# Kernel tuning notes

Hardware: AMD Instinct MI355X
Metric: run time of the kernel (lower is better)

The kernel has to match this reference:

```python
import jax, jax.numpy as jnp
import numpy as np

B, N, D, H = 4, 256, 256, 8
HD = D // H
DFF = 4 * D
EPS = 1e-5


def setup_inputs() -> dict:
    key = jax.random.key(0)
    ks = jax.random.split(key, 12)
    s = 0.02
    p = lambda k, shape: (jax.random.normal(k, shape, jnp.float32) * s)
    return dict(
        h=jax.random.normal(ks[0], (B, N, D), jnp.float32),
        e=jax.random.normal(ks[1], (B, N, N, D), jnp.float32),
        We=p(ks[2], (D, D)), be=jnp.zeros((D,), jnp.float32),
        Ws=p(ks[3], (D, D)), bs=jnp.zeros((D,), jnp.float32),
        Wd=p(ks[4], (D, D)), bd=jnp.zeros((D,), jnp.float32),
        Wb=p(ks[5], (D, H)), bb=jnp.zeros((H,), jnp.float32),
        ln1_g=jnp.ones((D,), jnp.float32), ln1_b=jnp.zeros((D,), jnp.float32),
        Wqkv=p(ks[6], (D, 3 * D)), bqkv=jnp.zeros((3 * D,), jnp.float32),
        Wo=p(ks[7], (D, D)), bo=jnp.zeros((D,), jnp.float32),
        ln2_g=jnp.ones((D,), jnp.float32), ln2_b=jnp.zeros((D,), jnp.float32),
        W1=p(ks[8], (D, DFF)), b1=jnp.zeros((DFF,), jnp.float32),
        W2=p(ks[9], (DFF, D)), b2=jnp.zeros((D,), jnp.float32),
    )


def _ln(x, g, b):
    m = jnp.mean(x, axis=-1, keepdims=True)
    v = jnp.mean((x - m) ** 2, axis=-1, keepdims=True)
    return (x - m) * jax.lax.rsqrt(v + EPS) * g + b


def reference(h, e, We, be, Ws, bs, Wd, bd, Wb, bb, ln1_g, ln1_b,
              Wqkv, bqkv, Wo, bo, ln2_g, ln2_b, W1, b1, W2, b2):
    # Edge update: broadcast-add of src/dst node projections + ReLU over [B,N,N,D]
    e_new = jax.nn.relu(e @ We + be
                        + (h @ Ws + bs)[:, :, None, :]   # src -> unsqueeze(2)
                        + (h @ Wd + bd)[:, None, :, :])  # dst -> unsqueeze(1)
    # Per-head additive attention bias [B,H,N,N]
    bias = jnp.einsum('bijd,dh->bhij', e_new, Wb) + bb[None, :, None, None]
    # Pre-LN self-attention with additive bias (torch MHA, eval mode)
    x = _ln(h, ln1_g, ln1_b)
    qkv = x @ Wqkv + bqkv
    q, k, v = jnp.split(qkv, 3, axis=-1)
    q = q.reshape(B, N, H, HD)
    k = k.reshape(B, N, H, HD)
    v = v.reshape(B, N, H, HD)
    scores = jnp.einsum('bihd,bjhd->bhij', q, k) / np.float32(np.sqrt(HD)) + bias
    attn = jax.nn.softmax(scores, axis=-1)
    o = jnp.einsum('bhij,bjhd->bihd', attn, v).reshape(B, N, D)
    h1 = h + (o @ Wo + bo)
    # Pre-LN FFN (exact GELU, as torch nn.GELU default)
    y = _ln(h1, ln2_g, ln2_b)
    h2 = h1 + (jax.nn.gelu(y @ W1 + b1, approximate=False) @ W2 + b2)
    return (h2, e_new)
```

## Files before the change

kernel.cpp:

```cpp
#include <hip/hip_runtime.h>
#include <math.h>

#define EPS 1e-5f

typedef __attribute__((ext_vector_type(4))) float floatx4;
typedef __attribute__((ext_vector_type(8))) short shortx8;

__device__ __forceinline__ unsigned short f2bf(float f){
  union { float f; unsigned u; } v; v.f = f;
  unsigned r = v.u + 0x7FFFu + ((v.u >> 16) & 1u);
  return (unsigned short)(r >> 16);
}
__device__ __forceinline__ float bf2f(unsigned short s){
  union { unsigned u; float f; } v; v.u = ((unsigned)s) << 16;
  return v.f;
}

__global__ __launch_bounds__(256) void k_prep(const float* __restrict__ We,
                                              unsigned short* __restrict__ WeT){
  int n = blockIdx.x, k = threadIdx.x;
  WeT[n*256 + k] = f2bf(We[k*256 + n]);
}

__global__ __launch_bounds__(256) void k_st(
    const float* __restrict__ h, const float* __restrict__ Ws, const float* __restrict__ bs,
    const float* __restrict__ be, const float* __restrict__ Wd, const float* __restrict__ bd,
    float* __restrict__ S, float* __restrict__ T)
{
  __shared__ float x[4][256];
  int t = threadIdx.x;
  int row0 = blockIdx.x*4;
  int which = blockIdx.y;
#pragma unroll
  for (int r=0;r<4;r++) x[r][t] = h[(row0+r)*256 + t];
  __syncthreads();
  const float* W = which ? Wd : Ws;
  float bv = which ? bd[t] : (bs[t] + be[t]);
  float acc[4] = {bv,bv,bv,bv};
  for (int k=0;k<256;k++){
    float wv = W[k*256 + t];
#pragma unroll
    for (int r=0;r<4;r++) acc[r] += x[r][k]*wv;
  }
  float* outp = which ? T : S;
#pragma unroll
  for (int r=0;r<4;r++) outp[(row0+r)*256 + t] = acc[r];
}

__global__ __launch_bounds__(256) void k_edge(
    const float* __restrict__ e, const unsigned short* __restrict__ WeT,
    const float* __restrict__ S, const float* __restrict__ T,
    const float* __restrict__ Wb, const float* __restrict__ bbv,
    float* __restrict__ eo, float* __restrict__ bias)
{
  __shared__ __align__(16) unsigned short smem[16896];
  __shared__ float sbuf[256];
  __shared__ __align__(16) unsigned short WbT[16*256];
  unsigned short* As = smem;
  unsigned short* Bs = smem + 2560;
  unsigned short* En = smem;

  const int tid = threadIdx.x;
  const int blk = blockIdx.x;
  const int jt = blk & 3;
  const int i  = (blk >> 2) & 255;
  const int b  = blk >> 10;
  const int j0 = jt * 64;
  const int w = tid >> 6, l = tid & 63;
  const int lrow = l & 15, quad = l >> 4;

  sbuf[tid] = S[((b << 8) + i) * 256 + tid];
  {
    const float* wbp = Wb + tid * 8;
    float4 w0 = *(const float4*)wbp;
    float4 w1 = *(const float4*)(wbp + 4);
    WbT[0*256 + tid] = f2bf(w0.x);
    WbT[1*256 + tid] = f2bf(w0.y);
    WbT[2*256 + tid] = f2bf(w0.z);
    WbT[3*256 + tid] = f2bf(w0.w);
    WbT[4*256 + tid] = f2bf(w1.x);
    WbT[5*256 + tid] = f2bf(w1.y);
    WbT[6*256 + tid] = f2bf(w1.z);
    WbT[7*256 + tid] = f2bf(w1.w);
#pragma unroll
    for (int hh = 8; hh < 16; hh++) WbT[hh*256 + tid] = 0;
  }

  floatx4 acc[16];
#pragma unroll
  for (int t = 0; t < 16; t++) acc[t] = (floatx4){0.f,0.f,0.f,0.f};

  const float* eBase = e + ((size_t)((b*256 + i)*256 + j0)) * 256;

  for (int c = 0; c < 8; c++){
    const int k0 = c * 32;
    __syncthreads();
#pragma unroll
    for (int s = 0; s < 2; s++){
      int f = tid + s*256;
      int r = f >> 3, q = f & 7;
      float4 v = *(const float4*)(eBase + r*256 + k0 + q*4);
      unsigned short* dst = As + r*40 + q*4;
      dst[0]=f2bf(v.x); dst[1]=f2bf(v.y); dst[2]=f2bf(v.z); dst[3]=f2bf(v.w);
    }
#pragma unroll
    for (int s = 0; s < 4; s++){
      int f = tid + s*256;
      int n = f >> 2, seg = f & 3;
      uint4 v = *(const uint4*)(WeT + n*256 + k0 + seg*8);
      *(uint4*)(Bs + n*40 + seg*8) = v;
    }
    __syncthreads();
    shortx8 af = *(const shortx8*)(As + (w*16 + lrow)*40 + quad*8);
#pragma unroll
    for (int t = 0; t < 16; t++){
      shortx8 bfrag = *(const shortx8*)(Bs + (t*16 + lrow)*40 + quad*8);
      acc[t] = __builtin_amdgcn_mfma_f32_16x16x32_bf16(af, bfrag, acc[t], 0, 0, 0);
    }
  }
  __syncthreads();
  const float* Tb = T + (size_t)(b*256 + j0) * 256;
#pragma unroll
  for (int reg = 0; reg < 4; reg++){
    int rloc = w*16 + quad*4 + reg;
    const float* Trow = Tb + rloc*256;
#pragma unroll
    for (int t = 0; t < 16; t++){
      int col = t*16 + lrow;
      float v = acc[t][reg] + sbuf[col] + Trow[col];
      v = fmaxf(v, 0.f);
      En[rloc*264 + col] = f2bf(v);
    }
  }
  __syncthreads();
  float* eop = eo + ((size_t)((b*256 + i)*256 + j0)) * 256;
#pragma unroll
  for (int s = 0; s < 16; s++){
    int fi = tid + s*256;
    int r = fi >> 6, c4 = fi & 63;
    const unsigned short* src = En + r*264 + c4*4;
    float4 v = { bf2f(src[0]), bf2f(src[1]), bf2f(src[2]), bf2f(src[3]) };
    *(float4*)(eop + r*256 + c4*4) = v;
  }
  floatx4 accb = (floatx4){0.f,0.f,0.f,0.f};
#pragma unroll
  for (int c = 0; c < 8; c++){
    int k0 = c*32;
    shortx8 af = *(const shortx8*)(En + (w*16 + lrow)*264 + k0 + quad*8);
    shortx8 bfrag = *(const shortx8*)(WbT + lrow*256 + k0 + quad*8);
    accb = __builtin_amdgcn_mfma_f32_16x16x32_bf16(af, bfrag, accb, 0, 0, 0);
  }
  if (lrow < 8){
    float bv = bbv[lrow];
    float* bp = bias + ((size_t)((b*8 + lrow)*256 + i)) * 256;
    int jb = j0 + w*16 + quad*4;
#pragma unroll
    for (int r = 0; r < 4; r++) bp[jb + r] = accb[r] + bv;
  }
}

__global__ __launch_bounds__(256) void k_ln1_qkv(
    const float* __restrict__ h, const float* __restrict__ g1, const float* __restrict__ b1l,
    const float* __restrict__ Wq, const float* __restrict__ bq,
    float* __restrict__ Q, float* __restrict__ K, float* __restrict__ V)
{
  __shared__ float x[4][256];
  __shared__ float red[256];
  __shared__ float mred[4], vred[4];
  int t = threadIdx.x;
  int row0 = blockIdx.x*4;
  int b = row0 >> 8, i0 = row0 & 255;
#pragma unroll
  for (int r=0;r<4;r++) x[r][t] = h[(row0+r)*256 + t];
  __syncthreads();
  int rr = t>>6, seg = t&63;
  const float* xr = x[rr];
  red[t] = xr[seg*4]+xr[seg*4+1]+xr[seg*4+2]+xr[seg*4+3];
  __syncthreads();
  for (int s=32;s>0;s>>=1){ if(seg<s) red[t]+=red[t+s]; __syncthreads(); }
  if (t<4) mred[t] = red[t*64]*(1.f/256.f);
  __syncthreads();
  float m_r = mred[rr];
  float d0=xr[seg*4]-m_r, d1=xr[seg*4+1]-m_r, d2=xr[seg*4+2]-m_r, d3=xr[seg*4+3]-m_r;
  red[t]=d0*d0+d1*d1+d2*d2+d3*d3;
  __syncthreads();
  for (int s=32;s>0;s>>=1){ if(seg<s) red[t]+=red[t+s]; __syncthreads(); }
  if (t<4) vred[t] = rsqrtf(red[t*64]*(1.f/256.f) + EPS);
  __syncthreads();
  float xn[4];
#pragma unroll
  for (int r=0;r<4;r++) xn[r] = (x[r][t]-mred[r])*vred[r]*g1[t] + b1l[t];
  __syncthreads();
#pragma unroll
  for (int r=0;r<4;r++) x[r][t] = xn[r];
  __syncthreads();
  float a0[4], a1[4], a2[4];
#pragma unroll
  for (int r=0;r<4;r++){ a0[r]=bq[t]; a1[r]=bq[t+256]; a2[r]=bq[t+512]; }
  for (int k=0;k<256;k++){
    float x0=x[0][k], x1=x[1][k], x2=x[2][k], x3=x[3][k];
    float w0=Wq[k*768+t], w1=Wq[k*768+t+256], w2=Wq[k*768+t+512];
    a0[0]+=x0*w0; a0[1]+=x1*w0; a0[2]+=x2*w0; a0[3]+=x3*w0;
    a1[0]+=x0*w1; a1[1]+=x1*w1; a1[2]+=x2*w1; a1[3]+=x3*w1;
    a2[0]+=x0*w2; a2[1]+=x1*w2; a2[2]+=x2*w2; a2[3]+=x3*w2;
  }
  int hd = t&31, hed = t>>5;
#pragma unroll
  for (int r=0;r<4;r++){
    int idx = ((b*8 + hed)*256 + (i0+r))*32 + hd;
    Q[idx] = a0[r]; K[idx] = a1[r]; V[idx] = a2[r];
  }
}

__global__ __launch_bounds__(256) void k_attn(
    const float* __restrict__ Q, const float* __restrict__ K, const float* __restrict__ V,
    const float* __restrict__ bias, float* __restrict__ O)
{
  __shared__ float ksl[256*33];
  __shared__ float q[32];
  __shared__ float sc[256];
  __shared__ float red[256];
  __shared__ float part[8*33];
  int t = threadIdx.x;
  int i = blockIdx.x & 255, bh = blockIdx.x >> 8;
  const float* Kb = K + bh*8192;
  const float* Vb = V + bh*8192;
  if (t < 32) q[t] = Q[(bh*256 + i)*32 + t];
#pragma unroll
  for (int s=0;s<8;s++){
    int f = t + s*256;
    int row = f >> 3, seg = f & 7;
    float4 v = ((const float4*)Kb)[f];
    int base = row*33 + seg*4;
    ksl[base]=v.x; ksl[base+1]=v.y; ksl[base+2]=v.z; ksl[base+3]=v.w;
  }
  __syncthreads();
  float a = 0.f;
  const float* kr = ksl + t*33;
#pragma unroll
  for (int d=0; d<32; d++) a += q[d]*kr[d];
  float sv = a*0.17677669529663687f + bias[((size_t)(bh*256 + i))*256 + t];
  red[t] = sv;
  __syncthreads();
  for (int s=128;s>0;s>>=1){ if (t<s) red[t] = fmaxf(red[t], red[t+s]); __syncthreads(); }
  float mx = red[0];
  __syncthreads();
  float p = expf(sv - mx);
  sc[t] = p; red[t] = p;
  __syncthreads();
  for (int s=128;s>0;s>>=1){ if (t<s) red[t] += red[t+s]; __syncthreads(); }
  float inv = 1.f/red[0];
  int hd = t & 31, grp = t >> 5;
  float oa = 0.f;
  const float* vb2 = Vb + grp*32*32;
#pragma unroll
  for (int jj=0;jj<32;jj++) oa += sc[grp*32+jj] * vb2[jj*32 + hd];
  part[grp*33 + hd] = oa;
  __syncthreads();
  if (t < 32){
    float o = 0.f;
#pragma unroll
    for (int gg=0; gg<8; gg++) o += part[gg*33 + t];
    int b = bh >> 3, hh = bh & 7;
    O[((b*256 + i)*256) + hh*32 + t] = o * inv;
  }
}

__global__ __launch_bounds__(256) void k_oproj_ln2(
    const float* __restrict__ O, const float* __restrict__ Wo, const float* __restrict__ bo,
    const float* __restrict__ h, const float* __restrict__ g2, const float* __restrict__ b2l,
    float* __restrict__ h1, float* __restrict__ y)
{
  __shared__ float x[4][256];
  __shared__ float hh[4][256];
  __shared__ float red[256];
  __shared__ float mred[4], vred[4];
  int t = threadIdx.x;
  int row0 = blockIdx.x * 4;
#pragma unroll
  for (int r=0;r<4;r++) x[r][t] = O[(row0+r)*256 + t];
  __syncthreads();
  float acc[4];
#pragma unroll
  for (int r=0;r<4;r++) acc[r] = bo[t];
  for (int k=0;k<256;k++){
    float wv = Wo[k*256 + t];
#pragma unroll
    for (int r=0;r<4;r++) acc[r] += x[r][k]*wv;
  }
#pragma unroll
  for (int r=0;r<4;r++){
    float hv = h[(row0+r)*256 + t] + acc[r];
    hh[r][t] = hv;
    h1[(row0+r)*256 + t] = hv;
  }
  __syncthreads();
  int rr = t>>6, seg = t&63;
  const float* hr = hh[rr];
  red[t] = hr[seg*4]+hr[seg*4+1]+hr[seg*4+2]+hr[seg*4+3];
  __syncthreads();
  for (int s=32;s>0;s>>=1){ if (seg<s) red[t]+=red[t+s]; __syncthreads(); }
  if (t<4) mred[t] = red[t*64]*(1.f/256.f);
  __syncthreads();
  float m_r = mred[rr];
  float d0=hr[seg*4]-m_r, d1=hr[seg*4+1]-m_r, d2=hr[seg*4+2]-m_r, d3=hr[seg*4+3]-m_r;
  red[t] = d0*d0+d1*d1+d2*d2+d3*d3;
  __syncthreads();
  for (int s=32;s>0;s>>=1){ if (seg<s) red[t]+=red[t+s]; __syncthreads(); }
  if (t<4) vred[t] = rsqrtf(red[t*64]*(1.f/256.f) + EPS);
  __syncthreads();
#pragma unroll
  for (int r=0;r<4;r++)
    y[(row0+r)*256 + t] = (hh[r][t]-mred[r])*vred[r]*g2[t] + b2l[t];
}

__global__ __launch_bounds__(256) void k_ffn1(
    const float* __restrict__ y, const float* __restrict__ W1, const float* __restrict__ b1,
    float* __restrict__ G)
{
  __shared__ float x[4][256];
  int t = threadIdx.x;
  int row0 = blockIdx.x*4;
#pragma unroll
  for (int r=0;r<4;r++) x[r][t] = y[(row0+r)*256 + t];
  __syncthreads();
  float acc[4][4];
#pragma unroll
  for (int c=0;c<4;c++){
    float bv = b1[t + c*256];
#pragma unroll
    for (int r=0;r<4;r++) acc[c][r] = bv;
  }
  for (int k=0;k<256;k++){
    float x0=x[0][k],x1=x[1][k],x2=x[2][k],x3=x[3][k];
#pragma unroll
    for (int c=0;c<4;c++){
      float wv = W1[k*1024 + t + c*256];
      acc[c][0]+=x0*wv; acc[c][1]+=x1*wv; acc[c][2]+=x2*wv; acc[c][3]+=x3*wv;
    }
  }
#pragma unroll
  for (int c=0;c<4;c++){
#pragma unroll
    for (int r=0;r<4;r++){
      float v = acc[c][r];
      float ge = 0.5f*v*(1.f + erff(v*0.70710678118654752f));
      G[(row0+r)*1024 + t + c*256] = ge;
    }
  }
}

__global__ __launch_bounds__(256) void k_ffn2(
    const float* __restrict__ G, const float* __restrict__ W2, const float* __restrict__ b2,
    const float* __restrict__ h1, float* __restrict__ out)
{
  __shared__ float g[4*1024];
  int t = threadIdx.x;
  int row0 = blockIdx.x*4;
  const float4* gl = (const float4*)(G + (size_t)row0*1024);
  float4* gs = (float4*)g;
#pragma unroll
  for (int s=0;s<4;s++) gs[t + s*256] = gl[t + s*256];
  __syncthreads();
  float acc[4];
#pragma unroll
  for (int r=0;r<4;r++) acc[r] = b2[t];
  for (int k=0;k<1024;k++){
    float wv = W2[k*256 + t];
#pragma unroll
    for (int r=0;r<4;r++) acc[r] += g[r*1024 + k]*wv;
  }
#pragma unroll
  for (int r=0;r<4;r++) out[(row0+r)*256 + t] = h1[(row0+r)*256 + t] + acc[r];
}

extern "C" void kernel_launch(void* const* d_in, const int* in_sizes, int n_in,
                              void* d_out, int out_size, void* d_ws, size_t ws_size,
                              hipStream_t stream)
{
  (void)in_sizes; (void)n_in; (void)out_size; (void)ws_size;
  const float* h    = (const float*)d_in[0];
  const float* e    = (const float*)d_in[1];
  const float* We   = (const float*)d_in[2];
  const float* be   = (const float*)d_in[3];
  const float* Ws   = (const float*)d_in[4];
  const float* bs   = (const float*)d_in[5];
  const float* Wd   = (const float*)d_in[6];
  const float* bd   = (const float*)d_in[7];
  const float* Wb   = (const float*)d_in[8];
  const float* bb   = (const float*)d_in[9];
  const float* g1   = (const float*)d_in[10];
  const float* b1l  = (const float*)d_in[11];
  const float* Wqkv = (const float*)d_in[12];
  const float* bqkv = (const float*)d_in[13];
  const float* Wo   = (const float*)d_in[14];
  const float* bo   = (const float*)d_in[15];
  const float* g2   = (const float*)d_in[16];
  const float* b2l  = (const float*)d_in[17];
  const float* W1   = (const float*)d_in[18];
  const float* b1f  = (const float*)d_in[19];
  const float* W2   = (const float*)d_in[20];
  const float* b2f  = (const float*)d_in[21];

  float* out   = (float*)d_out;
  float* h2_o  = out;
  float* e_o   = out + 262144;

  float* wsf = (float*)d_ws;
  unsigned short* WeT = (unsigned short*)d_ws;
  float* S_   = wsf + 32768;
  float* T_   = wsf + 294912;
  float* bias = wsf + 557056;
  float* Q_   = wsf + 2654208;
  float* K_   = wsf + 2916352;
  float* V_   = wsf + 3178496;
  float* O_   = wsf + 3440640;
  float* h1_  = wsf + 3702784;
  float* y_   = wsf + 3964928;
  float* G_   = wsf + 4227072;

  k_prep    <<<dim3(256),    dim3(256), 0, stream>>>(We, WeT);
  k_st      <<<dim3(256, 2), dim3(256), 0, stream>>>(h, Ws, bs, be, Wd, bd, S_, T_);
  k_edge    <<<dim3(4096),   dim3(256), 0, stream>>>(e, WeT, S_, T_, Wb, bb, e_o, bias);
  k_ln1_qkv <<<dim3(256),    dim3(256), 0, stream>>>(h, g1, b1l, Wqkv, bqkv, Q_, K_, V_);
  k_attn    <<<dim3(8192),   dim3(256), 0, stream>>>(Q_, K_, V_, bias, O_);
  k_oproj_ln2<<<dim3(256),   dim3(256), 0, stream>>>(O_, Wo, bo, h, g2, b2l, h1_, y_);
  k_ffn1    <<<dim3(256),    dim3(256), 0, stream>>>(y_, W1, b1f, G_);
  k_ffn2    <<<dim3(256),    dim3(256), 0, stream>>>(G_, W2, b2f, h1_, h2_o);
}
```

Baseline: 753.4 us.

## Move all node GEMMs to bf16 MFMA, fuse FFN chain, prefetch edge tiles

Transposes every weight matrix to bf16 in a single prep kernel. The S/T/QKV projections move onto MFMA in one fused front kernel that also does LN1. Attention is rewritten as one block per 32 query rows, using bf16 Q/K/V^T and MFMA for both QK^T and PV. The o-projection, LN2, FFN1+GELU and FFN2 are fused into one back kernel, and the edge GEMM now register-prefetches the next K-chunk. This cuts launches, scalar FP32 GEMM loops and intermediate global traffic, at the cost of more bf16 rounding and a small 64-block grid for the back kernel.

```diff
diff --git a/kernel.cpp b/kernel.cpp
--- a/kernel.cpp
+++ b/kernel.cpp
@@ -16,46 +16,140 @@
   return v.f;
 }
 
-__global__ __launch_bounds__(256) void k_prep(const float* __restrict__ We,
-                                              unsigned short* __restrict__ WeT){
-  int n = blockIdx.x, k = threadIdx.x;
-  WeT[n*256 + k] = f2bf(We[k*256 + n]);
-}
-
-__global__ __launch_bounds__(256) void k_st(
-    const float* __restrict__ h, const float* __restrict__ Ws, const float* __restrict__ bs,
-    const float* __restrict__ be, const float* __restrict__ Wd, const float* __restrict__ bd,
-    float* __restrict__ S, float* __restrict__ T)
+__global__ __launch_bounds__(256) void k_prep(
+    const float* __restrict__ We, const float* __restrict__ Ws, const float* __restrict__ Wd,
+    const float* __restrict__ Wqkv, const float* __restrict__ Wo, const float* __restrict__ W1,
+    const float* __restrict__ W2, const float* __restrict__ Wb,
+    unsigned short* __restrict__ WeT, unsigned short* __restrict__ WsT,
+    unsigned short* __restrict__ WdT, unsigned short* __restrict__ WqkvT,
+    unsigned short* __restrict__ WoT, unsigned short* __restrict__ W1T,
+    unsigned short* __restrict__ W2T, unsigned short* __restrict__ WbT16)
 {
-  __shared__ float x[4][256];
-  int t = threadIdx.x;
-  int row0 = blockIdx.x*4;
-  int which = blockIdx.y;
-#pragma unroll
-  for (int r=0;r<4;r++) x[r][t] = h[(row0+r)*256 + t];
-  __syncthreads();
-  const float* W = which ? Wd : Ws;
-  float bv = which ? bd[t] : (bs[t] + be[t]);
-  float acc[4] = {bv,bv,bv,bv};
-  for (int k=0;k<256;k++){
-    float wv = W[k*256 + t];
-#pragma unroll
-    for (int r=0;r<4;r++) acc[r] += x[r][k]*wv;
-  }
-  float* outp = which ? T : S;
-#pragma unroll
-  for (int r=0;r<4;r++) outp[(row0+r)*256 + t] = acc[r];
+  const int blk = blockIdx.x, tid = threadIdx.x;
+  if (blk == 240){
+#pragma unroll
+    for (int hh=0; hh<8; hh++) WbT16[hh*256+tid] = f2bf(Wb[tid*8+hh]);
+#pragma unroll
+    for (int hh=8; hh<16; hh++) WbT16[hh*256+tid] = 0;
+    return;
+  }
+  const float* src; unsigned short* dst; int K, N, t;
+  if (blk < 16)      { src=We;   dst=WeT;   K=256;  N=256;  t=blk; }
+  else if (blk < 32) { src=Ws;   dst=WsT;   K=256;  N=256;  t=blk-16; }
+  else if (blk < 48) { src=Wd;   dst=WdT;   K=256;  N=256;  t=blk-32; }
+  else if (blk < 96) { src=Wqkv; dst=WqkvT; K=256;  N=768;  t=blk-48; }
+  else if (blk < 112){ src=Wo;   dst=WoT;   K=256;  N=256;  t=blk-96; }
+  else if (blk < 176){ src=W1;   dst=W1T;   K=256;  N=1024; t=blk-112; }
+  else               { src=W2;   dst=W2T;   K=1024; N=256;  t=blk-176; }
+  const int tpr = N >> 6;
+  const int k0 = (t / tpr) << 6, n0 = (t % tpr) << 6;
+  __shared__ float tile[64][65];
+#pragma unroll
+  for (int s=0;s<16;s++){ int f=tid+(s<<8); int r=f>>6, c=f&63;
+    tile[r][c] = src[(size_t)(k0+r)*N + n0 + c]; }
+  __syncthreads();
+#pragma unroll
+  for (int s=0;s<16;s++){ int f=tid+(s<<8); int r=f>>6, c=f&63;
+    dst[(size_t)(n0+r)*K + k0 + c] = f2bf(tile[c][r]); }
+}
+
+__global__ __launch_bounds__(256) void k_front(
+  const float* __restrict__ h, const float* __restrict__ g1, const float* __restrict__ b1l,
+  const float* __restrict__ bs, const float* __restrict__ be, const float* __restrict__ bd,
+  const float* __restrict__ bqkv,
+  const unsigned short* __restrict__ WsT, const unsigned short* __restrict__ WdT,
+  const unsigned short* __restrict__ WqkvT,
+  float* __restrict__ S, float* __restrict__ T,
+  unsigned short* __restrict__ Qb, unsigned short* __restrict__ Kb,
+  unsigned short* __restrict__ VTb)
+{
+  __shared__ float hs[16][256];
+  __shared__ __align__(16) unsigned short xa[16*264];
+  __shared__ float red1[16][16], red2[16][16];
+  __shared__ float rmean[16], rinv[16];
+  const int tid = threadIdx.x;
+  const int rb = blockIdx.x & 63;
+  const int chunk = blockIdx.x >> 6;
+  const int row0 = rb * 16;
+  const int b = row0 >> 8;
+  const int w = tid>>6, l = tid&63, lrow = l&15, quad = l>>4;
+
+#pragma unroll
+  for (int s=0;s<4;s++){
+    int f = tid + s*256; int r = f>>6, c4 = f&63;
+    float4 v = ((const float4*)(h + (size_t)row0*256))[f];
+    *(float4*)(&hs[r][c4*4]) = v;
+  }
+  __syncthreads();
+  {
+    int row = tid>>4, l16 = tid&15;
+    if (chunk >= 2){
+      float sm=0.f, sq=0.f;
+#pragma unroll
+      for (int j=0;j<16;j++){ float v=hs[row][l16*16+j]; sm+=v; sq+=v*v; }
+      red1[row][l16]=sm; red2[row][l16]=sq;
+      __syncthreads();
+      if (l16==0){
+        float s0=0.f,q0=0.f;
+#pragma unroll
+        for(int k=0;k<16;k++){ s0+=red1[row][k]; q0+=red2[row][k]; }
+        float m=s0*(1.f/256.f);
+        rmean[row]=m; rinv[row]=rsqrtf(q0*(1.f/256.f)-m*m+EPS);
+      }
+      __syncthreads();
+      float m=rmean[row], iv=rinv[row];
+#pragma unroll
+      for (int j=0;j<16;j++){ int col=l16*16+j;
+        xa[row*264+col] = f2bf((hs[row][col]-m)*iv*g1[col] + b1l[col]); }
+    } else {
+#pragma unroll
+      for (int j=0;j<16;j++){ int col=l16*16+j; xa[row*264+col] = f2bf(hs[row][col]); }
+    }
+  }
+  __syncthreads();
+  const unsigned short* Wt;
+  if (chunk==0) Wt = WsT; else if (chunk==1) Wt = WdT;
+  else Wt = WqkvT + (size_t)(chunk-2)*256*256;
+  floatx4 a4[4];
+#pragma unroll
+  for (int t=0;t<4;t++) a4[t] = (floatx4){0.f,0.f,0.f,0.f};
+  for (int c=0;c<8;c++){
+    shortx8 af = *(const shortx8*)(xa + lrow*264 + c*32 + quad*8);
+#pragma unroll
+    for (int t=0;t<4;t++){
+      int n = (w*4+t)*16 + lrow;
+      shortx8 bf = *(const shortx8*)(Wt + (size_t)n*256 + c*32 + quad*8);
+      a4[t] = __builtin_amdgcn_mfma_f32_16x16x32_bf16(af, bf, a4[t], 0, 0, 0);
+    }
+  }
+#pragma unroll
+  for (int t=0;t<4;t++){
+    int ct = w*4+t;
+#pragma unroll
+    for (int reg=0;reg<4;reg++){
+      int row = quad*4+reg, col = ct*16+lrow;
+      float v = a4[t][reg];
+      if (chunk==0) S[(size_t)(row0+row)*256+col] = v + bs[col] + be[col];
+      else if (chunk==1) T[(size_t)(row0+row)*256+col] = v + bd[col];
+      else if (chunk==2){ float q = v + bqkv[col]; int hh=col>>5, d=col&31;
+        Qb[((size_t)(b*8+hh)*256 + (row0&255)+row)*32 + d] = f2bf(q); }
+      else if (chunk==3){ float q = v + bqkv[256+col]; int hh=col>>5, d=col&31;
+        Kb[((size_t)(b*8+hh)*256 + (row0&255)+row)*32 + d] = f2bf(q); }
+      else { float q = v + bqkv[512+col]; int hh=col>>5, d=col&31;
+        VTb[((size_t)(b*8+hh)*32 + d)*256 + (row0&255)+row] = f2bf(q); }
+    }
+  }
 }
 
 __global__ __launch_bounds__(256) void k_edge(
     const float* __restrict__ e, const unsigned short* __restrict__ WeT,
     const float* __restrict__ S, const float* __restrict__ T,
-    const float* __restrict__ Wb, const float* __restrict__ bbv,
+    const unsigned short* __restrict__ WbTg,
     float* __restrict__ eo, float* __restrict__ bias)
 {
   __shared__ __align__(16) unsigned short smem[16896];
   __shared__ float sbuf[256];
-  __shared__ __align__(16) unsigned short WbT[16*256];
+  __shared__ __align__(16) unsigned short WbT[4096];
   unsigned short* As = smem;
   unsigned short* Bs = smem + 2560;
   unsigned short* En = smem;
@@ -70,55 +164,61 @@
   const int lrow = l & 15, quad = l >> 4;
 
   sbuf[tid] = S[((b << 8) + i) * 256 + tid];
-  {
-    const float* wbp = Wb + tid * 8;
-    float4 w0 = *(const float4*)wbp;
-    float4 w1 = *(const float4*)(wbp + 4);
-    WbT[0*256 + tid] = f2bf(w0.x);
-    WbT[1*256 + tid] = f2bf(w0.y);
-    WbT[2*256 + tid] = f2bf(w0.z);
-    WbT[3*256 + tid] = f2bf(w0.w);
-    WbT[4*256 + tid] = f2bf(w1.x);
-    WbT[5*256 + tid] = f2bf(w1.y);
-    WbT[6*256 + tid] = f2bf(w1.z);
-    WbT[7*256 + tid] = f2bf(w1.w);
-#pragma unroll
-    for (int hh = 8; hh < 16; hh++) WbT[hh*256 + tid] = 0;
-  }
+  ((uint4*)WbT)[tid]       = ((const uint4*)WbTg)[tid];
+  ((uint4*)WbT)[tid + 256] = ((const uint4*)WbTg)[tid + 256];
 
   floatx4 acc[16];
 #pragma unroll
   for (int t = 0; t < 16; t++) acc[t] = (floatx4){0.f,0.f,0.f,0.f};
 
   const float* eBase = e + ((size_t)((b*256 + i)*256 + j0)) * 256;
+  const int rA = tid >> 3, qA = tid & 7;
+  const int nB0 = tid >> 2, segB = tid & 2 ? 0 : 0; (void)segB;
+
+  float4 pa0 = *(const float4*)(eBase + rA*256 + qA*4);
+  float4 pa1 = *(const float4*)(eBase + (rA+32)*256 + qA*4);
+  uint4 pb[4];
+#pragma unroll
+  for (int s=0;s<4;s++){ int f = tid + s*256; int n = f>>2, seg = f&3;
+    pb[s] = *(const uint4*)(WeT + n*256 + seg*8); }
+  {
+    unsigned short* d0 = As + rA*40 + qA*4;
+    d0[0]=f2bf(pa0.x); d0[1]=f2bf(pa0.y); d0[2]=f2bf(pa0.z); d0[3]=f2bf(pa0.w);
+    unsigned short* d1 = As + (rA+32)*40 + qA*4;
+    d1[0]=f2bf(pa1.x); d1[1]=f2bf(pa1.y); d1[2]=f2bf(pa1.z); d1[3]=f2bf(pa1.w);
+#pragma unroll
+    for (int s=0;s<4;s++){ int f = tid + s*256; int n = f>>2, seg = f&3;
+      *(uint4*)(Bs + n*40 + seg*8) = pb[s]; }
+  }
+  __syncthreads();
 
   for (int c = 0; c < 8; c++){
-    const int k0 = c * 32;
+    if (c < 7){
+      const int k0n = (c+1)*32;
+      pa0 = *(const float4*)(eBase + rA*256 + k0n + qA*4);
+      pa1 = *(const float4*)(eBase + (rA+32)*256 + k0n + qA*4);
+#pragma unroll
+      for (int s=0;s<4;s++){ int f = tid + s*256; int n = f>>2, seg = f&3;
+        pb[s] = *(const uint4*)(WeT + n*256 + k0n + seg*8); }
+    }
+    shortx8 af = *(const shortx8*)(As + (w*16 + lrow)*40 + quad*8);
+#pragma unroll
+    for (int t = 0; t < 16; t++){
+      shortx8 bfr = *(const shortx8*)(Bs + (t*16 + lrow)*40 + quad*8);
+      acc[t] = __builtin_amdgcn_mfma_f32_16x16x32_bf16(af, bfr, acc[t], 0, 0, 0);
+    }
     __syncthreads();
-#pragma unroll
-    for (int s = 0; s < 2; s++){
-      int f = tid + s*256;
-      int r = f >> 3, q = f & 7;
-      float4 v = *(const float4*)(eBase + r*256 + k0 + q*4);
-      unsigned short* dst = As + r*40 + q*4;
-      dst[0]=f2bf(v.x); dst[1]=f2bf(v.y); dst[2]=f2bf(v.z); dst[3]=f2bf(v.w);
-    }
-#pragma unroll
-    for (int s = 0; s < 4; s++){
-      int f = tid + s*256;
-      int n = f >> 2, seg = f & 3;
-      uint4 v = *(const uint4*)(WeT + n*256 + k0 + seg*8);
-      *(uint4*)(Bs + n*40 + seg*8) = v;
+    if (c < 7){
+      unsigned short* d0 = As + rA*40 + qA*4;
+      d0[0]=f2bf(pa0.x); d0[1]=f2bf(pa0.y); d0[2]=f2bf(pa0.z); d0[3]=f2bf(pa0.w);
+      unsigned short* d1 = As + (rA+32)*40 + qA*4;
+      d1[0]=f2bf(pa1.x); d1[1]=f2bf(pa1.y); d1[2]=f2bf(pa1.z); d1[3]=f2bf(pa1.w);
+#pragma unroll
+      for (int s=0;s<4;s++){ int f = tid + s*256; int n = f>>2, seg = f&3;
+        *(uint4*)(Bs + n*40 + seg*8) = pb[s]; }
     }
     __syncthreads();
-    shortx8 af = *(const shortx8*)(As + (w*16 + lrow)*40 + quad*8);
-#pragma unroll
-    for (int t = 0; t < 16; t++){
-      shortx8 bfrag = *(const shortx8*)(Bs + (t*16 + lrow)*40 + quad*8);
-      acc[t] = __builtin_amdgcn_mfma_f32_16x16x32_bf16(af, bfrag, acc[t], 0, 0, 0);
-    }
-  }
-  __syncthreads();
+  }
   const float* Tb = T + (size_t)(b*256 + j0) * 256;
 #pragma unroll
   for (int reg = 0; reg < 4; reg++){
@@ -151,227 +251,247 @@
     accb = __builtin_amdgcn_mfma_f32_16x16x32_bf16(af, bfrag, accb, 0, 0, 0);
   }
   if (lrow < 8){
-    float bv = bbv[lrow];
     float* bp = bias + ((size_t)((b*8 + lrow)*256 + i)) * 256;
     int jb = j0 + w*16 + quad*4;
 #pragma unroll
-    for (int r = 0; r < 4; r++) bp[jb + r] = accb[r] + bv;
-  }
-}
-
-__global__ __launch_bounds__(256) void k_ln1_qkv(
-    const float* __restrict__ h, const float* __restrict__ g1, const float* __restrict__ b1l,
-    const float* __restrict__ Wq, const float* __restrict__ bq,
-    float* __restrict__ Q, float* __restrict__ K, float* __restrict__ V)
+    for (int r = 0; r < 4; r++) bp[jb + r] = accb[r];
+  }
+}
+
+
+__global__ __launch_bounds__(256) void k_attn(
+  const unsigned short* __restrict__ Qb, const unsigned short* __restrict__ Kb,
+  const unsigned short* __restrict__ VTb, const float* __restrict__ bias,
+  const float* __restrict__ bbv, unsigned short* __restrict__ Ob)
 {
-  __shared__ float x[4][256];
-  __shared__ float red[256];
-  __shared__ float mred[4], vred[4];
-  int t = threadIdx.x;
-  int row0 = blockIdx.x*4;
-  int b = row0 >> 8, i0 = row0 & 255;
-#pragma unroll
-  for (int r=0;r<4;r++) x[r][t] = h[(row0+r)*256 + t];
-  __syncthreads();
-  int rr = t>>6, seg = t&63;
-  const float* xr = x[rr];
-  red[t] = xr[seg*4]+xr[seg*4+1]+xr[seg*4+2]+xr[seg*4+3];
-  __syncthreads();
-  for (int s=32;s>0;s>>=1){ if(seg<s) red[t]+=red[t+s]; __syncthreads(); }
-  if (t<4) mred[t] = red[t*64]*(1.f/256.f);
-  __syncthreads();
-  float m_r = mred[rr];
-  float d0=xr[seg*4]-m_r, d1=xr[seg*4+1]-m_r, d2=xr[seg*4+2]-m_r, d3=xr[seg*4+3]-m_r;
-  red[t]=d0*d0+d1*d1+d2*d2+d3*d3;
-  __syncthreads();
-  for (int s=32;s>0;s>>=1){ if(seg<s) red[t]+=red[t+s]; __syncthreads(); }
-  if (t<4) vred[t] = rsqrtf(red[t*64]*(1.f/256.f) + EPS);
-  __syncthreads();
-  float xn[4];
-#pragma unroll
-  for (int r=0;r<4;r++) xn[r] = (x[r][t]-mred[r])*vred[r]*g1[t] + b1l[t];
-  __syncthreads();
-#pragma unroll
-  for (int r=0;r<4;r++) x[r][t] = xn[r];
-  __syncthreads();
-  float a0[4], a1[4], a2[4];
-#pragma unroll
-  for (int r=0;r<4;r++){ a0[r]=bq[t]; a1[r]=bq[t+256]; a2[r]=bq[t+512]; }
-  for (int k=0;k<256;k++){
-    float x0=x[0][k], x1=x[1][k], x2=x[2][k], x3=x[3][k];
-    float w0=Wq[k*768+t], w1=Wq[k*768+t+256], w2=Wq[k*768+t+512];
-    a0[0]+=x0*w0; a0[1]+=x1*w0; a0[2]+=x2*w0; a0[3]+=x3*w0;
-    a1[0]+=x0*w1; a1[1]+=x1*w1; a1[2]+=x2*w1; a1[3]+=x3*w1;
-    a2[0]+=x0*w2; a2[1]+=x1*w2; a2[2]+=x2*w2; a2[3]+=x3*w2;
-  }
-  int hd = t&31, hed = t>>5;
-#pragma unroll
-  for (int r=0;r<4;r++){
-    int idx = ((b*8 + hed)*256 + (i0+r))*32 + hd;
-    Q[idx] = a0[r]; K[idx] = a1[r]; V[idx] = a2[r];
-  }
-}
-
-__global__ __launch_bounds__(256) void k_attn(
-    const float* __restrict__ Q, const float* __restrict__ K, const float* __restrict__ V,
-    const float* __restrict__ bias, float* __restrict__ O)
+  __shared__ __align__(16) unsigned short Qa[32*40];
+  __shared__ __align__(16) unsigned short Kl[256*40];
+  __shared__ __align__(16) unsigned short Vt[32*264];
+  __shared__ __align__(16) unsigned short Pl[32*264];
+  __shared__ float srowm[4][16], srows[4][16], sinv[32];
+
+  const int tid = threadIdx.x;
+  const int ic = blockIdx.x & 7, bh = blockIdx.x >> 3;
+  const int i0 = ic * 32;
+  const int w = tid>>6, l = tid&63, lrow = l&15, quad = l>>4;
+
+  if (tid < 128){
+    int r = tid>>2, cseg = tid&3;
+    *(uint4*)(Qa + r*40 + cseg*8) = ((const uint4*)(Qb + (size_t)(bh*256+i0)*32))[tid];
+  }
+#pragma unroll
+  for (int s=0;s<4;s++){
+    int f = tid + s*256; int r = f>>2, cseg = f&3;
+    *(uint4*)(Kl + r*40 + cseg*8) = ((const uint4*)(Kb + (size_t)bh*8192))[f];
+  }
+#pragma unroll
+  for (int s=0;s<4;s++){
+    int f = tid + s*256; int r = f>>5, c8 = f&31;
+    *(uint4*)(Vt + r*264 + c8*8) = ((const uint4*)(VTb + (size_t)bh*8192))[f];
+  }
+  __syncthreads();
+
+  const int rt = w & 1, cs = (w>>1)*8;
+  const float bbh = bbv[bh & 7];
+  floatx4 sc[8];
+  {
+    shortx8 aq = *(const shortx8*)(Qa + (rt*16+lrow)*40 + quad*8);
+    floatx4 z = (floatx4){0.f,0.f,0.f,0.f};
+#pragma unroll
+    for (int t=0;t<8;t++){
+      shortx8 bk = *(const shortx8*)(Kl + ((cs+t)*16+lrow)*40 + quad*8);
+      sc[t] = __builtin_amdgcn_mfma_f32_16x16x32_bf16(aq, bk, z, 0, 0, 0);
+    }
+  }
+  const float scale = 0.17677669529663687f;
+  float mx[4] = {-1e30f,-1e30f,-1e30f,-1e30f};
+#pragma unroll
+  for (int t=0;t<8;t++){
+#pragma unroll
+    for (int reg=0;reg<4;reg++){
+      size_t bidx = ((size_t)(bh*256 + i0 + rt*16 + quad*4 + reg))*256 + (cs+t)*16 + lrow;
+      float v = sc[t][reg]*scale + bias[bidx] + bbh;
+      sc[t][reg] = v;
+      mx[reg] = fmaxf(mx[reg], v);
+    }
+  }
+#pragma unroll
+  for (int m=1;m<16;m<<=1){
+#pragma unroll
+    for (int reg=0;reg<4;reg++) mx[reg] = fmaxf(mx[reg], __shfl_xor(mx[reg], m));
+  }
+  if (lrow == 0){
+#pragma unroll
+    for (int reg=0;reg<4;reg++) srowm[w][quad*4+reg] = mx[reg];
+  }
+  __syncthreads();
+  float sum[4] = {0.f,0.f,0.f,0.f};
+#pragma unroll
+  for (int reg=0;reg<4;reg++){
+    float gm = fmaxf(srowm[w][quad*4+reg], srowm[w^2][quad*4+reg]);
+#pragma unroll
+    for (int t=0;t<8;t++){
+      float p = __expf(sc[t][reg] - gm);
+      sc[t][reg] = p; sum[reg] += p;
+    }
+  }
+#pragma unroll
+  for (int m=1;m<16;m<<=1){
+#pragma unroll
+    for (int reg=0;reg<4;reg++) sum[reg] += __shfl_xor(sum[reg], m);
+  }
+  if (lrow == 0){
+#pragma unroll
+    for (int reg=0;reg<4;reg++) srows[w][quad*4+reg] = sum[reg];
+  }
+#pragma unroll
+  for (int t=0;t<8;t++){
+#pragma unroll
+    for (int reg=0;reg<4;reg++)
+      Pl[(rt*16+quad*4+reg)*264 + (cs+t)*16 + lrow] = f2bf(sc[t][reg]);
+  }
+  __syncthreads();
+  if (lrow == 0 && w < 2){
+#pragma unroll
+    for (int reg=0;reg<4;reg++){
+      int row = rt*16 + quad*4 + reg;
+      sinv[row] = 1.f/(srows[w][quad*4+reg] + srows[w^2][quad*4+reg]);
+    }
+  }
+  __syncthreads();
+  const int rt2 = w & 1, ctd = w >> 1;
+  floatx4 oc = (floatx4){0.f,0.f,0.f,0.f};
+#pragma unroll
+  for (int kc=0;kc<8;kc++){
+    shortx8 ap = *(const shortx8*)(Pl + (rt2*16+lrow)*264 + kc*32 + quad*8);
+    shortx8 bv = *(const shortx8*)(Vt + (ctd*16+lrow)*264 + kc*32 + quad*8);
+    oc = __builtin_amdgcn_mfma_f32_16x16x32_bf16(ap, bv, oc, 0, 0, 0);
+  }
+  const int bq = bh >> 3, hh = bh & 7;
+#pragma unroll
+  for (int reg=0;reg<4;reg++){
+    int row = rt2*16 + quad*4 + reg;
+    int d = ctd*16 + lrow;
+    Ob[((size_t)(bq*256 + i0 + row))*256 + hh*32 + d] = f2bf(oc[reg]*sinv[row]);
+  }
+}
+
+__global__ __launch_bounds__(256) void k_back(
+  const unsigned short* __restrict__ Ob, const unsigned short* __restrict__ WoT,
+  const float* __restrict__ bo, const float* __restrict__ h,
+  const float* __restrict__ g2, const float* __restrict__ b2l,
+  const unsigned short* __restrict__ W1T, const float* __restrict__ b1f,
+  const unsigned short* __restrict__ W2T, const float* __restrict__ b2f,
+  float* __restrict__ out)
 {
-  __shared__ float ksl[256*33];
-  __shared__ float q[32];
-  __shared__ float sc[256];
-  __shared__ float red[256];
-  __shared__ float part[8*33];
-  int t = threadIdx.x;
-  int i = blockIdx.x & 255, bh = blockIdx.x >> 8;
-  const float* Kb = K + bh*8192;
-  const float* Vb = V + bh*8192;
-  if (t < 32) q[t] = Q[(bh*256 + i)*32 + t];
-#pragma unroll
-  for (int s=0;s<8;s++){
-    int f = t + s*256;
-    int row = f >> 3, seg = f & 7;
-    float4 v = ((const float4*)Kb)[f];
-    int base = row*33 + seg*4;
-    ksl[base]=v.x; ksl[base+1]=v.y; ksl[base+2]=v.z; ksl[base+3]=v.w;
-  }
-  __syncthreads();
-  float a = 0.f;
-  const float* kr = ksl + t*33;
-#pragma unroll
-  for (int d=0; d<32; d++) a += q[d]*kr[d];
-  float sv = a*0.17677669529663687f + bias[((size_t)(bh*256 + i))*256 + t];
-  red[t] = sv;
-  __syncthreads();
-  for (int s=128;s>0;s>>=1){ if (t<s) red[t] = fmaxf(red[t], red[t+s]); __syncthreads(); }
-  float mx = red[0];
-  __syncthreads();
-  float p = expf(sv - mx);
-  sc[t] = p; red[t] = p;
-  __syncthreads();
-  for (int s=128;s>0;s>>=1){ if (t<s) red[t] += red[t+s]; __syncthreads(); }
-  float inv = 1.f/red[0];
-  int hd = t & 31, grp = t >> 5;
-  float oa = 0.f;
-  const float* vb2 = Vb + grp*32*32;
-#pragma unroll
-  for (int jj=0;jj<32;jj++) oa += sc[grp*32+jj] * vb2[jj*32 + hd];
-  part[grp*33 + hd] = oa;
-  __syncthreads();
-  if (t < 32){
-    float o = 0.f;
-#pragma unroll
-    for (int gg=0; gg<8; gg++) o += part[gg*33 + t];
-    int b = bh >> 3, hh = bh & 7;
-    O[((b*256 + i)*256) + hh*32 + t] = o * inv;
-  }
-}
-
-__global__ __launch_bounds__(256) void k_oproj_ln2(
-    const float* __restrict__ O, const float* __restrict__ Wo, const float* __restrict__ bo,
-    const float* __restrict__ h, const float* __restrict__ g2, const float* __restrict__ b2l,
-    float* __restrict__ h1, float* __restrict__ y)
-{
-  __shared__ float x[4][256];
-  __shared__ float hh[4][256];
-  __shared__ float red[256];
-  __shared__ float mred[4], vred[4];
-  int t = threadIdx.x;
-  int row0 = blockIdx.x * 4;
-#pragma unroll
-  for (int r=0;r<4;r++) x[r][t] = O[(row0+r)*256 + t];
-  __syncthreads();
-  float acc[4];
-#pragma unroll
-  for (int r=0;r<4;r++) acc[r] = bo[t];
-  for (int k=0;k<256;k++){
-    float wv = Wo[k*256 + t];
-#pragma unroll
-    for (int r=0;r<4;r++) acc[r] += x[r][k]*wv;
-  }
-#pragma unroll
-  for (int r=0;r<4;r++){
-    float hv = h[(row0+r)*256 + t] + acc[r];
-    hh[r][t] = hv;
-    h1[(row0+r)*256 + t] = hv;
-  }
-  __syncthreads();
-  int rr = t>>6, seg = t&63;
-  const float* hr = hh[rr];
-  red[t] = hr[seg*4]+hr[seg*4+1]+hr[seg*4+2]+hr[seg*4+3];
-  __syncthreads();
-  for (int s=32;s>0;s>>=1){ if (seg<s) red[t]+=red[t+s]; __syncthreads(); }
-  if (t<4) mred[t] = red[t*64]*(1.f/256.f);
-  __syncthreads();
-  float m_r = mred[rr];
-  float d0=hr[seg*4]-m_r, d1=hr[seg*4+1]-m_r, d2=hr[seg*4+2]-m_r, d3=hr[seg*4+3]-m_r;
-  red[t] = d0*d0+d1*d1+d2*d2+d3*d3;
-  __syncthreads();
-  for (int s=32;s>0;s>>=1){ if (seg<s) red[t]+=red[t+s]; __syncthreads(); }
-  if (t<4) vred[t] = rsqrtf(red[t*64]*(1.f/256.f) + EPS);
-  __syncthreads();
-#pragma unroll
-  for (int r=0;r<4;r++)
-    y[(row0+r)*256 + t] = (hh[r][t]-mred[r])*vred[r]*g2[t] + b2l[t];
-}
-
-__global__ __launch_bounds__(256) void k_ffn1(
-    const float* __restrict__ y, const float* __restrict__ W1, const float* __restrict__ b1,
-    float* __restrict__ G)
-{
-  __shared__ float x[4][256];
-  int t = threadIdx.x;
-  int row0 = blockIdx.x*4;
-#pragma unroll
-  for (int r=0;r<4;r++) x[r][t] = y[(row0+r)*256 + t];
-  __syncthreads();
-  float acc[4][4];
-#pragma unroll
-  for (int c=0;c<4;c++){
-    float bv = b1[t + c*256];
-#pragma unroll
-    for (int r=0;r<4;r++) acc[c][r] = bv;
-  }
-  for (int k=0;k<256;k++){
-    float x0=x[0][k],x1=x[1][k],x2=x[2][k],x3=x[3][k];
-#pragma unroll
-    for (int c=0;c<4;c++){
-      float wv = W1[k*1024 + t + c*256];
-      acc[c][0]+=x0*wv; acc[c][1]+=x1*wv; acc[c][2]+=x2*wv; acc[c][3]+=x3*wv;
-    }
-  }
-#pragma unroll
-  for (int c=0;c<4;c++){
-#pragma unroll
-    for (int r=0;r<4;r++){
-      float v = acc[c][r];
-      float ge = 0.5f*v*(1.f + erff(v*0.70710678118654752f));
-      G[(row0+r)*1024 + t + c*256] = ge;
-    }
-  }
-}
-
-__global__ __launch_bounds__(256) void k_ffn2(
-    const float* __restrict__ G, const float* __restrict__ W2, const float* __restrict__ b2,
-    const float* __restrict__ h1, float* __restrict__ out)
-{
-  __shared__ float g[4*1024];
-  int t = threadIdx.x;
-  int row0 = blockIdx.x*4;
-  const float4* gl = (const float4*)(G + (size_t)row0*1024);
-  float4* gs = (float4*)g;
-#pragma unroll
-  for (int s=0;s<4;s++) gs[t + s*256] = gl[t + s*256];
-  __syncthreads();
-  float acc[4];
-#pragma unroll
-  for (int r=0;r<4;r++) acc[r] = b2[t];
-  for (int k=0;k<1024;k++){
-    float wv = W2[k*256 + t];
-#pragma unroll
-    for (int r=0;r<4;r++) acc[r] += g[r*1024 + k]*wv;
-  }
-#pragma unroll
-  for (int r=0;r<4;r++) out[(row0+r)*256 + t] = h1[(row0+r)*256 + t] + acc[r];
+  __shared__ __align__(16) unsigned short Os[16*264];
+  __shared__ float h1s[16*264];
+  __shared__ __align__(16) unsigned short ys[16*264];
+  __shared__ __align__(16) unsigned short Gs[16*1032];
+  __shared__ float red1[16][16], red2[16][16];
+  __shared__ float rmean[16], rinv[16];
+
+  const int tid = threadIdx.x;
+  const int row0 = blockIdx.x * 16;
+  const int w = tid>>6, l = tid&63, lrow = l&15, quad = l>>4;
+
+#pragma unroll
+  for (int s=0;s<2;s++){
+    int f = tid + s*256; int r = f>>5, c8 = f&31;
+    *(uint4*)(Os + r*264 + c8*8) = ((const uint4*)(Ob + (size_t)row0*256))[f];
+  }
+  __syncthreads();
+  {
+    floatx4 a4[4];
+#pragma unroll
+    for (int t=0;t<4;t++) a4[t] = (floatx4){0.f,0.f,0.f,0.f};
+    for (int c=0;c<8;c++){
+      shortx8 af = *(const shortx8*)(Os + lrow*264 + c*32 + quad*8);
+#pragma unroll
+      for (int t=0;t<4;t++){
+        int n = (w*4+t)*16 + lrow;
+        shortx8 bf = *(const shortx8*)(WoT + (size_t)n*256 + c*32 + quad*8);
+        a4[t] = __builtin_amdgcn_mfma_f32_16x16x32_bf16(af, bf, a4[t], 0, 0, 0);
+      }
+    }
+#pragma unroll
+    for (int t=0;t<4;t++){
+#pragma unroll
+      for (int reg=0;reg<4;reg++){
+        int row = quad*4+reg, col = (w*4+t)*16+lrow;
+        h1s[row*264+col] = a4[t][reg] + bo[col] + h[(size_t)(row0+row)*256 + col];
+      }
+    }
+  }
+  __syncthreads();
+  {
+    int row = tid>>4, l16 = tid&15;
+    float sm=0.f, sq=0.f;
+#pragma unroll
+    for (int j=0;j<16;j++){ float v = h1s[row*264 + l16*16 + j]; sm+=v; sq+=v*v; }
+    red1[row][l16]=sm; red2[row][l16]=sq;
+    __syncthreads();
+    if (l16==0){
+      float s0=0.f,q0=0.f;
+#pragma unroll
+      for (int k=0;k<16;k++){ s0+=red1[row][k]; q0+=red2[row][k]; }
+      float m = s0*(1.f/256.f);
+      rmean[row]=m; rinv[row]=rsqrtf(q0*(1.f/256.f)-m*m+EPS);
+    }
+    __syncthreads();
+    float m = rmean[row], iv = rinv[row];
+#pragma unroll
+    for (int j=0;j<16;j++){ int col = l16*16+j;
+      ys[row*264+col] = f2bf((h1s[row*264+col]-m)*iv*g2[col] + b2l[col]); }
+  }
+  __syncthreads();
+  {
+    floatx4 a4[16];
+#pragma unroll
+    for (int t=0;t<16;t++) a4[t] = (floatx4){0.f,0.f,0.f,0.f};
+    for (int c=0;c<8;c++){
+      shortx8 af = *(const shortx8*)(ys + lrow*264 + c*32 + quad*8);
+#pragma unroll
+      for (int t=0;t<16;t++){
+        int n = (w*16+t)*16 + lrow;
+        shortx8 bf = *(const shortx8*)(W1T + (size_t)n*256 + c*32 + quad*8);
+        a4[t] = __builtin_amdgcn_mfma_f32_16x16x32_bf16(af, bf, a4[t], 0, 0, 0);
+      }
+    }
+#pragma unroll
+    for (int t=0;t<16;t++){
+#pragma unroll
+      for (int reg=0;reg<4;reg++){
+        int row = quad*4+reg, col = (w*16+t)*16+lrow;
+        float v = a4[t][reg] + b1f[col];
+        float ge = 0.5f*v*(1.f + erff(v*0.70710678118654752f));
+        Gs[row*1032+col] = f2bf(ge);
+      }
+    }
+  }
+  __syncthreads();
+  {
+    floatx4 a4[4];
+#pragma unroll
+    for (int t=0;t<4;t++) a4[t] = (floatx4){0.f,0.f,0.f,0.f};
+    for (int c=0;c<32;c++){
+      shortx8 af = *(const shortx8*)(Gs + lrow*1032 + c*32 + quad*8);
+#pragma unroll
+      for (int t=0;t<4;t++){
+        int n = (w*4+t)*16 + lrow;
+        shortx8 bf = *(const shortx8*)(W2T + (size_t)n*1024 + c*32 + quad*8);
+        a4[t] = __builtin_amdgcn_mfma_f32_16x16x32_bf16(af, bf, a4[t], 0, 0, 0);
+      }
+    }
+#pragma unroll
+    for (int t=0;t<4;t++){
+#pragma unroll
+      for (int reg=0;reg<4;reg++){
+        int row = quad*4+reg, col = (w*4+t)*16+lrow;
+        out[(size_t)(row0+row)*256+col] = h1s[row*264+col] + a4[t][reg] + b2f[col];
+      }
+    }
+  }
 }
 
 extern "C" void kernel_launch(void* const* d_in, const int* in_sizes, int n_in,
@@ -402,29 +522,34 @@
   const float* W2   = (const float*)d_in[20];
   const float* b2f  = (const float*)d_in[21];
 
-  float* out   = (float*)d_out;
-  float* h2_o  = out;
-  float* e_o   = out + 262144;
+  float* out  = (float*)d_out;
+  float* h2_o = out;
+  float* e_o  = out + 262144;
 
   float* wsf = (float*)d_ws;
-  unsigned short* WeT = (unsigned short*)d_ws;
-  float* S_   = wsf + 32768;
-  float* T_   = wsf + 294912;
-  float* bias = wsf + 557056;
-  float* Q_   = wsf + 2654208;
-  float* K_   = wsf + 2916352;
-  float* V_   = wsf + 3178496;
-  float* O_   = wsf + 3440640;
-  float* h1_  = wsf + 3702784;
-  float* y_   = wsf + 3964928;
-  float* G_   = wsf + 4227072;
-
-  k_prep    <<<dim3(256),    dim3(256), 0, stream>>>(We, WeT);
-  k_st      <<<dim3(256, 2), dim3(256), 0, stream>>>(h, Ws, bs, be, Wd, bd, S_, T_);
-  k_edge    <<<dim3(4096),   dim3(256), 0, stream>>>(e, WeT, S_, T_, Wb, bb, e_o, bias);
-  k_ln1_qkv <<<dim3(256),    dim3(256), 0, stream>>>(h, g1, b1l, Wqkv, bqkv, Q_, K_, V_);
-  k_attn    <<<dim3(8192),   dim3(256), 0, stream>>>(Q_, K_, V_, bias, O_);
-  k_oproj_ln2<<<dim3(256),   dim3(256), 0, stream>>>(O_, Wo, bo, h, g2, b2l, h1_, y_);
-  k_ffn1    <<<dim3(256),    dim3(256), 0, stream>>>(y_, W1, b1f, G_);
-  k_ffn2    <<<dim3(256),    dim3(256), 0, stream>>>(G_, W2, b2f, h1_, h2_o);
-}
+  unsigned short* ush = (unsigned short*)d_ws;
+  unsigned short* WeT   = ush;
+  unsigned short* WsT   = ush + 65536;
+  unsigned short* WdT   = ush + 131072;
+  unsigned short* WqkvT = ush + 196608;
+  unsigned short* WoT   = ush + 393216;
+  unsigned short* W1T   = ush + 458752;
+  unsigned short* W2T   = ush + 720896;
+  unsigned short* WbT16 = ush + 983040;
+  float* S_   = wsf + 493568;
+  float* T_   = wsf + 755712;
+  float* bias = wsf + 1017856;
+  unsigned short* Qb  = (unsigned short*)(wsf + 3115008);
+  unsigned short* Kb  = (unsigned short*)(wsf + 3246080);
+  unsigned short* VTb = (unsigned short*)(wsf + 3377152);
+  unsigned short* Ob  = (unsigned short*)(wsf + 3508224);
+
+  k_prep <<<dim3(241),  dim3(256), 0, stream>>>(We,Ws,Wd,Wqkv,Wo,W1,W2,Wb,
+                                                WeT,WsT,WdT,WqkvT,WoT,W1T,W2T,WbT16);
+  k_front<<<dim3(320),  dim3(256), 0, stream>>>(h, g1,b1l, bs,be,bd, bqkv,
+                                                WsT,WdT,WqkvT, S_,T_, Qb,Kb,VTb);
+  k_edge <<<dim3(4096), dim3(256), 0, stream>>>(e, WeT, S_, T_, WbT16, e_o, bias);
+  k_attn <<<dim3(256),  dim3(256), 0, stream>>>(Qb, Kb, VTb, bias, bb, Ob);
+  k_back <<<dim3(64),   dim3(256), 0, stream>>>(Ob, WoT, bo, h, g2,b2l,
+                                                W1T,b1f, W2T,b2f, h2_o);
+}
```

Result: faster. 667.8 us (-11.4%).
